# Optimization experiments

Measured on AMD Instinct MI355X. Metric: run time of the kernel, lower is better.

Reference implementation:

```python
import jax, jax.numpy as jnp
import numpy as np

N = 50000   # nodes
E = 800000  # edges (before self-loops)
D = 96      # hidden_dim (= per-head out_channels, concat=False averages heads)
H = 4       # heads
L = 2       # num_layers
NEG_SLOPE = 0.2
EPS_BN = 1e-5


def setup_inputs() -> dict:
    key = jax.random.key(0)
    ks = jax.random.split(key, 8)
    x = jax.random.normal(ks[0], (N, D), dtype=jnp.float32)
    edge_index = jax.random.randint(ks[1], (2, E), 0, N, dtype=jnp.int64)
    # GATConv shared lin: in D -> H*D (per-head dim D), Glorot-ish scale
    W = jax.random.normal(ks[2], (L, D, H * D), dtype=jnp.float32) / np.sqrt(D).astype(np.float32)
    att_src = jax.random.normal(ks[3], (L, H, D), dtype=jnp.float32) * 0.1
    att_dst = jax.random.normal(ks[4], (L, H, D), dtype=jnp.float32) * 0.1
    bias = jnp.zeros((L, D), dtype=jnp.float32)
    gamma = jnp.ones((L, D), dtype=jnp.float32)
    beta = jnp.zeros((L, D), dtype=jnp.float32)
    return dict(x=x, edge_index=edge_index, W=W, att_src=att_src,
                att_dst=att_dst, bias=bias, gamma=gamma, beta=beta)


def _gat_layer(x, src, dst, W, a_src, a_dst, b):
    h = (x @ W).reshape(N, H, D)                      # [N,H,D]
    alpha_src = jnp.einsum('nhd,hd->nh', h, a_src)    # [N,H]
    alpha_dst = jnp.einsum('nhd,hd->nh', h, a_dst)    # [N,H]
    e = jax.nn.leaky_relu(alpha_src[src] + alpha_dst[dst], NEG_SLOPE)  # [Etot,H]
    # edge softmax grouped by destination node (numerically stable)
    m = jax.ops.segment_max(e, dst, num_segments=N)   # [N,H]
    p = jnp.exp(e - m[dst])
    denom = jax.ops.segment_sum(p, dst, num_segments=N)
    alpha = p / (denom[dst] + 1e-16)                  # [Etot,H]
    msg = h[src] * alpha[:, :, None]                  # [Etot,H,D]
    out = jax.ops.segment_sum(msg, dst, num_segments=N)  # [N,H,D]
    return out.mean(axis=1) + b                       # concat=False -> head mean


def reference(x, edge_index, W, att_src, att_dst, bias, gamma, beta):
    # PyG GATConv adds self-loops by default
    loops = jnp.arange(N, dtype=edge_index.dtype)
    ei = jnp.concatenate([edge_index, jnp.stack([loops, loops])], axis=1)
    src, dst = ei[0], ei[1]
    for l in range(L):
        x_res = x
        out = _gat_layer(x, src, dst, W[l], att_src[l], att_dst[l], bias[l])
        # BatchNorm over nodes (training-mode batch statistics, biased var)
        mu = out.mean(axis=0)
        var = out.var(axis=0)
        out = (out - mu) / jnp.sqrt(var + EPS_BN) * gamma[l] + beta[l]
        # dropout is identity at inference
        x = jax.nn.relu(out) + x_res
    return x
```

## Files before the change

kernel.cpp:

```cpp
#include <hip/hip_runtime.h>

#define DD 96
#define HH 4
#define HD 384
#define GN 32
#define NEG_SLOPE 0.2f
#define NB_STATS 128
#define SCAN_BS 1024

typedef unsigned int uint;
typedef unsigned short ushort;

__device__ inline uint pack2bf(float lo, float hi) {
    uint ulo = __float_as_uint(lo); ulo += 0x7fffu + ((ulo >> 16) & 1u);
    uint uhi = __float_as_uint(hi); uhi += 0x7fffu + ((uhi >> 16) & 1u);
    return (ulo >> 16) | (uhi & 0xffff0000u);
}

__global__ void wa_kernel(const float* __restrict__ W, const float* __restrict__ att_src,
                          const float* __restrict__ att_dst, float* __restrict__ wa) {
    const int l = blockIdx.x / DD;
    const int k = blockIdx.x % DD;
    const int t = threadIdx.x;
    const float* Wr = W + ((size_t)l * DD + k) * HD;
    const float* as = att_src + (size_t)l * HD;
    const float* ad = att_dst + (size_t)l * HD;
    const bool hiHalf = t >= 32;
    float s0=0,s1=0,s2=0,s3=0,d0=0,d1=0,d2=0,d3=0;
    int c; float w, ps, pd;
    c = t;       w = Wr[c]; s0 = fmaf(w, as[c], s0); d0 = fmaf(w, ad[c], d0);
    c = t + 64;  w = Wr[c]; ps = w * as[c]; pd = w * ad[c];
    s0 += hiHalf ? 0.f : ps;  s1 += hiHalf ? ps : 0.f;
    d0 += hiHalf ? 0.f : pd;  d1 += hiHalf ? pd : 0.f;
    c = t + 128; w = Wr[c]; s1 = fmaf(w, as[c], s1); d1 = fmaf(w, ad[c], d1);
    c = t + 192; w = Wr[c]; s2 = fmaf(w, as[c], s2); d2 = fmaf(w, ad[c], d2);
    c = t + 256; w = Wr[c]; ps = w * as[c]; pd = w * ad[c];
    s2 += hiHalf ? 0.f : ps;  s3 += hiHalf ? ps : 0.f;
    d2 += hiHalf ? 0.f : pd;  d3 += hiHalf ? pd : 0.f;
    c = t + 320; w = Wr[c]; s3 = fmaf(w, as[c], s3); d3 = fmaf(w, ad[c], d3);
#pragma unroll
    for (int off = 32; off; off >>= 1) {
        s0 += __shfl_xor(s0, off); s1 += __shfl_xor(s1, off);
        s2 += __shfl_xor(s2, off); s3 += __shfl_xor(s3, off);
        d0 += __shfl_xor(d0, off); d1 += __shfl_xor(d1, off);
        d2 += __shfl_xor(d2, off); d3 += __shfl_xor(d3, off);
    }
    if (t == 0) {
        float* o = wa + ((size_t)l * DD + k) * 8;
        o[0]=s0; o[1]=d0; o[2]=s1; o[3]=d1; o[4]=s2; o[5]=d2; o[6]=s3; o[7]=d3;
    }
}

__global__ void __launch_bounds__(256) gemm_kernel(const float* __restrict__ x,
        const float* __restrict__ W, const float* __restrict__ wa,
        uint* __restrict__ hp, float* __restrict__ asrc, float* __restrict__ adst, int N) {
    __shared__ float xs[GN * 100];
    __shared__ float was[DD * 8];
    const int t = threadIdx.x;
    const int n0 = blockIdx.x * GN;
    const int nvalid = min(GN, N - n0);

    for (int i = t; i < DD * 8; i += 256) was[i] = wa[i];
    {
        const float4* xsrc = (const float4*)(x + (size_t)n0 * DD);
        const int lim = (nvalid * DD) / 4;
        for (int i4 = t; i4 < lim; i4 += 256) {
            const float4 v = xsrc[i4];
            const int node = i4 / 24, k = (i4 % 24) * 4;
            float* dp = &xs[node * 100 + k];
            dp[0] = v.x; dp[1] = v.y; dp[2] = v.z; dp[3] = v.w;
        }
    }
    __syncthreads();

    const int lane = t & 63;
    const int nb = (t >> 6) * 8;
    float acc[8][6];
#pragma unroll
    for (int nn = 0; nn < 8; nn++)
#pragma unroll
        for (int j = 0; j < 6; j++) acc[nn][j] = 0.f;

    for (int k = 0; k < DD; k++) {
        float wv[6];
#pragma unroll
        for (int j = 0; j < 6; j++) wv[j] = W[(size_t)k * HD + j * 64 + lane];
#pragma unroll
        for (int nn = 0; nn < 8; nn++) {
            const float xv = xs[(nb + nn) * 100 + k];
#pragma unroll
            for (int j = 0; j < 6; j++) acc[nn][j] = fmaf(xv, wv[j], acc[nn][j]);
        }
    }
#pragma unroll
    for (int nn = 0; nn < 8; nn++) {
        if (nb + nn < nvalid) {
            uint* hr = hp + (size_t)(n0 + nb + nn) * 192;
            hr[lane]       = pack2bf(acc[nn][0], acc[nn][1]);
            hr[64 + lane]  = pack2bf(acc[nn][2], acc[nn][3]);
            hr[128 + lane] = pack2bf(acc[nn][4], acc[nn][5]);
        }
    }
    {
        const int nn = t >> 3, j = t & 7;
        if (nn < nvalid) {
            const float* xr = &xs[nn * 100];
            float s = 0.f;
            for (int k = 0; k < DD; k++) s = fmaf(xr[k], was[k * 8 + j], s);
            const int n = n0 + nn, h = j >> 1;
            if ((j & 1) == 0) asrc[n * 4 + h] = s;
            else              adst[n * 4 + h] = s;
        }
    }
}

__global__ void count_kernel(const int* __restrict__ ei, int* __restrict__ deg, int E) {
    int i = blockIdx.x * blockDim.x + threadIdx.x;
    const int stride = gridDim.x * blockDim.x;
    for (; i < E; i += stride) atomicAdd(&deg[ei[E + i]], 1);
}

__global__ void scan1_kernel(const int* __restrict__ deg, int* __restrict__ locpre,
                             int* __restrict__ bsum, int N) {
    __shared__ int ts[256];
    const int t = threadIdx.x;
    const int base = blockIdx.x * SCAN_BS + t * 4;
    int e0 = 0, e1 = 0, e2 = 0, e3 = 0;
    if (base + 3 < N) {
        const int4 v = *(const int4*)(deg + base);
        e0 = v.x + 1; e1 = v.y + 1; e2 = v.z + 1; e3 = v.w + 1;
    } else {
        if (base     < N) e0 = deg[base]     + 1;
        if (base + 1 < N) e1 = deg[base + 1] + 1;
        if (base + 2 < N) e2 = deg[base + 2] + 1;
        if (base + 3 < N) e3 = deg[base + 3] + 1;
    }
    const int s = e0 + e1 + e2 + e3;
    ts[t] = s;
    __syncthreads();
    for (int off = 1; off < 256; off <<= 1) {
        const int u = (t >= off) ? ts[t - off] : 0;
        __syncthreads();
        ts[t] += u;
        __syncthreads();
    }
    const int ex = ts[t] - s;
    if (base + 3 < N) {
        *(int4*)(locpre + base) = make_int4(ex, ex + e0, ex + e0 + e1, ex + e0 + e1 + e2);
    } else if (base < N) {
        locpre[base] = ex;
        if (base + 1 < N) locpre[base + 1] = ex + e0;
        if (base + 2 < N) locpre[base + 2] = ex + e0 + e1;
    }
    if (t == 255) bsum[blockIdx.x] = ts[255];
}

__global__ void scan2_kernel(int* __restrict__ bsum, int* __restrict__ rowptr,
                             int NBLK, int N) {
    const int t = threadIdx.x;
    const int mine = (t < NBLK) ? bsum[t] : 0;
    int v = mine;
#pragma unroll
    for (int off = 1; off < 64; off <<= 1) {
        const int u = __shfl_up(v, off);
        if (t >= off) v += u;
    }
    if (t < NBLK) bsum[t] = v - mine;
    if (t == 63) rowptr[N] = v;
}

__global__ void scan3_kernel(const int* __restrict__ locpre, const int* __restrict__ bsum,
                             int* __restrict__ rowptr, int* __restrict__ cursor, int N) {
    const int base = blockIdx.x * SCAN_BS + threadIdx.x * 4;
    const int boff = bsum[blockIdx.x];
    if (base + 3 < N) {
        int4 v = *(const int4*)(locpre + base);
        v.x += boff; v.y += boff; v.z += boff; v.w += boff;
        *(int4*)(rowptr + base) = v;
        *(int4*)(cursor + base) = v;
    } else {
        for (int i = base; i < N; i++) {
            const int r = locpre[i] + boff;
            rowptr[i] = r; cursor[i] = r;
        }
    }
}

__global__ void scatter_kernel(const int* __restrict__ ei, int* __restrict__ cursor,
                               const int* __restrict__ rowptr, int* __restrict__ col,
                               int* __restrict__ dstarr, int E, int Etot) {
    int i = blockIdx.x * blockDim.x + threadIdx.x;
    const int stride = gridDim.x * blockDim.x;
    for (; i < Etot; i += stride) {
        if (i < E) {
            const int src = ei[i], dst = ei[E + i];
            const int pos = atomicAdd(&cursor[dst], 1);
            col[pos] = src;
            dstarr[pos] = dst;
        } else {
            const int n = i - E;
            const int pos = rowptr[n + 1] - 1;
            col[pos] = n;
            dstarr[pos] = n;
        }
    }
}

__global__ void ew_kernel(const int* __restrict__ col, const int* __restrict__ dstarr,
                          const float* __restrict__ asrc, const float* __restrict__ adst,
                          float4* __restrict__ ew4, int Etot) {
    int i = blockIdx.x * blockDim.x + threadIdx.x;
    const int stride = gridDim.x * blockDim.x;
    for (; i < Etot; i += stride) {
        const int s = col[i], d = dstarr[i];
        const float4 av = ((const float4*)asrc)[s];
        const float4 dv = ((const float4*)adst)[d];
        float e0 = av.x + dv.x, e1 = av.y + dv.y, e2 = av.z + dv.z, e3 = av.w + dv.w;
        e0 = e0 > 0.f ? e0 : NEG_SLOPE * e0;
        e1 = e1 > 0.f ? e1 : NEG_SLOPE * e1;
        e2 = e2 > 0.f ? e2 : NEG_SLOPE * e2;
        e3 = e3 > 0.f ? e3 : NEG_SLOPE * e3;
        ew4[i] = make_float4(__expf(e0), __expf(e1), __expf(e2), __expf(e3));
    }
}

__global__ void den_kernel(const int* __restrict__ rowptr, const float4* __restrict__ ew4,
                           float4* __restrict__ rden, int N) {
    const int n = blockIdx.x * blockDim.x + threadIdx.x;
    if (n >= N) return;
    const int beg = rowptr[n], endp = rowptr[n + 1];
    float s0 = 0.f, s1 = 0.f, s2 = 0.f, s3 = 0.f;
    for (int i = beg; i < endp; i++) {
        const float4 w = ew4[i];
        s0 += w.x; s1 += w.y; s2 += w.z; s3 += w.w;
    }
    rden[n] = make_float4(0.25f / (s0 + 1e-16f), 0.25f / (s1 + 1e-16f),
                          0.25f / (s2 + 1e-16f), 0.25f / (s3 + 1e-16f));
}

#define EDGE_FMA(u0, u1, u2, w4)                                                      \
    { const float cf1 = hi32 ? w4.y : w4.x;                                           \
      const float cf4 = hi32 ? w4.w : w4.z;                                           \
      acc0 = fmaf(__uint_as_float(u0 << 16), w4.x, acc0);                             \
      acc1 = fmaf(__uint_as_float(u0 & 0xffff0000u), cf1, acc1);                      \
      acc2 = fmaf(__uint_as_float(u1 << 16), w4.y, acc2);                             \
      acc3 = fmaf(__uint_as_float(u1 & 0xffff0000u), w4.z, acc3);                     \
      acc4 = fmaf(__uint_as_float(u2 << 16), cf4, acc4);                              \
      acc5 = fmaf(__uint_as_float(u2 & 0xffff0000u), w4.w, acc5); }

__global__ void agg_csr_kernel(const int* __restrict__ rowptr, const int* __restrict__ col,
                               const uint* __restrict__ hp, const float4* __restrict__ ew4,
                               const float4* __restrict__ rden, const float* __restrict__ bias,
                               float* __restrict__ y, int N) {
    const int lane = threadIdx.x & 63;
    const bool hi32 = lane >= 32;
    const int n = (blockIdx.x * blockDim.x + threadIdx.x) >> 6;
    if (n >= N) return;
    const int beg = rowptr[n], endp = rowptr[n + 1];
    float acc0=0,acc1=0,acc2=0,acc3=0,acc4=0,acc5=0;
    int e = beg;
    for (; e + 4 <= endp; e += 4) {
        const int s0 = col[e], s1 = col[e + 1], s2 = col[e + 2], s3 = col[e + 3];
        const float4 wA = ew4[e],     wB = ew4[e + 1];
        const float4 wC = ew4[e + 2], wD = ew4[e + 3];
        const uint* h0 = hp + (size_t)s0 * 192 + lane;
        const uint* h1 = hp + (size_t)s1 * 192 + lane;
        const uint* h2 = hp + (size_t)s2 * 192 + lane;
        const uint* h3 = hp + (size_t)s3 * 192 + lane;
        const uint u00 = h0[0], u01 = h0[64], u02 = h0[128];
        const uint u10 = h1[0], u11 = h1[64], u12 = h1[128];
        const uint u20 = h2[0], u21 = h2[64], u22 = h2[128];
        const uint u30 = h3[0], u31 = h3[64], u32 = h3[128];
        EDGE_FMA(u00, u01, u02, wA);
        EDGE_FMA(u10, u11, u12, wB);
        EDGE_FMA(u20, u21, u22, wC);
        EDGE_FMA(u30, u31, u32, wD);
    }
    for (; e < endp; e++) {
        const int s0 = col[e];
        const float4 wA = ew4[e];
        const uint* h0 = hp + (size_t)s0 * 192 + lane;
        const uint u00 = h0[0], u01 = h0[64], u02 = h0[128];
        EDGE_FMA(u00, u01, u02, wA);
    }
    const float4 rd = rden[n];
    const float rc1 = hi32 ? rd.y : rd.x;
    const float rc4 = hi32 ? rd.w : rd.z;
    const float A = acc0 * rd.x + acc3 * rd.z;
    const float B = acc1 * rc1  + acc4 * rc4;
    const float C = acc2 * rd.y + acc5 * rd.w;
    const float shB = __shfl_xor(B, 32);
    const float shC = __shfl_xor(C, 32);
    float* yr = y + (size_t)n * DD;
    yr[lane] = A + (hi32 ? shC : shB) + bias[lane];
    if (!hi32) yr[64 + lane] = B + shC + bias[64 + lane];
}

__global__ void bnstats_kernel(const float* __restrict__ y, float* __restrict__ pbuf,
                               int total4) {
    __shared__ float ps[384 * 4];
    __shared__ float qs[384 * 4];
    const int t = threadIdx.x;
    const int stride = gridDim.x * 384;
    float s0=0,s1=0,s2=0,s3=0,q0=0,q1=0,q2=0,q3=0;
    for (int i = blockIdx.x * 384 + t; i < total4; i += stride) {
        const float4 v = ((const float4*)y)[i];
        s0 += v.x; q0 = fmaf(v.x, v.x, q0);
        s1 += v.y; q1 = fmaf(v.y, v.y, q1);
        s2 += v.z; q2 = fmaf(v.z, v.z, q2);
        s3 += v.w; q3 = fmaf(v.w, v.w, q3);
    }
    ps[t*4+0]=s0; ps[t*4+1]=s1; ps[t*4+2]=s2; ps[t*4+3]=s3;
    qs[t*4+0]=q0; qs[t*4+1]=q1; qs[t*4+2]=q2; qs[t*4+3]=q3;
    __syncthreads();
    if (t < 192) {
        const int d = t % 96;
        const float* src = (t < 96) ? ps : qs;
        float r = 0.f;
#pragma unroll
        for (int m = 0; m < 16; m++) r += src[d + 96 * m];
        pbuf[blockIdx.x * 192 + t] = r;
    }
}

__global__ void bnfin_kernel(const float* __restrict__ pbuf, const float* __restrict__ gamma,
                             const float* __restrict__ beta, float* __restrict__ scsh, int N) {
    const int d = threadIdx.x;
    float s = 0.f, q = 0.f;
    for (int b = 0; b < NB_STATS; b++) {
        s += pbuf[b * 192 + d];
        q += pbuf[b * 192 + 96 + d];
    }
    const float invN = 1.f / (float)N;
    const float mu = s * invN;
    const float var = q * invN - mu * mu;
    const float sc = gamma[d] * rsqrtf(var + 1e-5f);
    scsh[d] = sc;
    scsh[d + DD] = beta[d] - mu * sc;
}

__global__ void bn_apply_kernel(const float* __restrict__ y, const float* __restrict__ scsh,
                                const float* __restrict__ xin, float* __restrict__ xout,
                                int total4) {
    int i = blockIdx.x * blockDim.x + threadIdx.x;
    const int stride = gridDim.x * blockDim.x;
    for (; i < total4; i += stride) {
        const int d4 = (i % 24) * 4;
        const float4 v = ((const float4*)y)[i];
        const float4 xi = ((const float4*)xin)[i];
        float4 o; float a;
        a = fmaf(v.x, scsh[d4],     scsh[d4 + DD]);     o.x = (a > 0.f ? a : 0.f) + xi.x;
        a = fmaf(v.y, scsh[d4 + 1], scsh[d4 + 1 + DD]); o.y = (a > 0.f ? a : 0.f) + xi.y;
        a = fmaf(v.z, scsh[d4 + 2], scsh[d4 + 2 + DD]); o.z = (a > 0.f ? a : 0.f) + xi.z;
        a = fmaf(v.w, scsh[d4 + 3], scsh[d4 + 3 + DD]); o.w = (a > 0.f ? a : 0.f) + xi.w;
        ((float4*)xout)[i] = o;
    }
}

extern "C" void kernel_launch(void* const* d_in, const int* in_sizes, int n_in,
                              void* d_out, int out_size, void* d_ws, size_t ws_size,
                              hipStream_t stream) {
    const float* x        = (const float*)d_in[0];
    const int*   ei       = (const int*)d_in[1];
    const float* W        = (const float*)d_in[2];
    const float* att_src  = (const float*)d_in[3];
    const float* att_dst  = (const float*)d_in[4];
    const float* bias     = (const float*)d_in[5];
    const float* gamma    = (const float*)d_in[6];
    const float* beta     = (const float*)d_in[7];
    float* out_final = (float*)d_out;

    const int N = in_sizes[0] / DD;
    const int E = in_sizes[1] / 2;
    const int Etot = E + N;
    const int NBLK = (N + SCAN_BS - 1) / SCAN_BS;

    char* ws = (char*)d_ws;
    size_t off = 0;
    auto alloc = [&](size_t bytes) -> void* {
        void* p = ws + off;
        off += (bytes + 255) & ~(size_t)255;
        return p;
    };
    uint*   hp     = (uint*)alloc((size_t)N * 192 * 4);
    float*  asrc   = (float*)alloc((size_t)N * HH * 4);
    float*  adst   = (float*)alloc((size_t)N * HH * 4);
    float*  y      = (float*)alloc((size_t)N * DD * 4);
    float*  xbuf   = (float*)alloc((size_t)N * DD * 4);
    float*  pbuf   = (float*)alloc((size_t)NB_STATS * 192 * 4);
    float*  scsh   = (float*)alloc(2 * DD * 4);
    float*  wa     = (float*)alloc(2 * DD * 8 * 4);
    int*    deg    = (int*)alloc((size_t)N * 4);
    int*    locpre = (int*)alloc((size_t)N * 4);
    int*    bsum   = (int*)alloc(64 * 4);
    int*    rowptr = (int*)alloc((size_t)(N + 1) * 4);
    int*    cursor = (int*)alloc((size_t)N * 4);
    int*    colidx = (int*)alloc((size_t)Etot * 4);
    int*    dstarr = (int*)alloc((size_t)Etot * 4);
    float4* ew4    = (float4*)alloc((size_t)Etot * 16);
    float4* rden   = (float4*)alloc((size_t)N * 16);

    hipMemsetAsync(deg, 0, (size_t)N * 4, stream);
    count_kernel<<<1024, 256, 0, stream>>>(ei, deg, E);
    scan1_kernel<<<NBLK, 256, 0, stream>>>(deg, locpre, bsum, N);
    scan2_kernel<<<1, 64, 0, stream>>>(bsum, rowptr, NBLK, N);
    scan3_kernel<<<NBLK, 256, 0, stream>>>(locpre, bsum, rowptr, cursor, N);
    scatter_kernel<<<1024, 256, 0, stream>>>(ei, cursor, rowptr, colidx, dstarr, E, Etot);
    wa_kernel<<<2 * DD, 64, 0, stream>>>(W, att_src, att_dst, wa);

    for (int l = 0; l < 2; l++) {
        const float* xin = (l == 0) ? x : xbuf;
        float* xout = (l == 1) ? out_final : xbuf;

        gemm_kernel<<<(N + GN - 1) / GN, 256, 0, stream>>>(
            xin, W + (size_t)l * DD * HD, wa + (size_t)l * DD * 8, hp, asrc, adst, N);
        ew_kernel<<<2048, 256, 0, stream>>>(colidx, dstarr, asrc, adst, ew4, Etot);
        den_kernel<<<(N + 255) / 256, 256, 0, stream>>>(rowptr, ew4, rden, N);
        agg_csr_kernel<<<(N * 64 + 255) / 256, 256, 0, stream>>>(
            rowptr, colidx, hp, ew4, rden, bias + (size_t)l * DD, y, N);
        bnstats_kernel<<<NB_STATS, 384, 0, stream>>>(y, pbuf, N * DD / 4);
        bnfin_kernel<<<1, DD, 0, stream>>>(pbuf, gamma + (size_t)l * DD,
                                           beta + (size_t)l * DD, scsh, N);
        bn_apply_kernel<<<2048, 256, 0, stream>>>(y, scsh, xin, xout, N * DD / 4);
    }
}
```

Baseline: 485.6 us.

## Fuse softmax denominator into aggregation and store bf16 features as contiguous triples

Removes the separate den_kernel: each aggregation wavefront now sums the edge weights itself while it gathers, so the per-node normalizer is computed in registers and the rden buffer and one launch per layer go away. The packed bf16 feature layout changes from three strided words per lane to three contiguous words per lane, written and read as a single 12-byte vector access. The gather loop unroll grows from 4 to 8 edges so more loads are in flight. The costs are redundant denominator adds across all 64 lanes, higher register pressure, and possibly less efficient unaligned 12-byte vector loads.

```diff
diff --git a/kernel.cpp b/kernel.cpp
--- a/kernel.cpp
+++ b/kernel.cpp
@@ -10,6 +10,9 @@
 
 typedef unsigned int uint;
 typedef unsigned short ushort;
+
+typedef uint uint3v __attribute__((ext_vector_type(3)));
+typedef uint3v __attribute__((aligned(4))) uint3a;
 
 __device__ inline uint pack2bf(float lo, float hi) {
     uint ulo = __float_as_uint(lo); ulo += 0x7fffu + ((ulo >> 16) & 1u);
@@ -95,10 +98,12 @@
 #pragma unroll
     for (int nn = 0; nn < 8; nn++) {
         if (nb + nn < nvalid) {
-            uint* hr = hp + (size_t)(n0 + nb + nn) * 192;
-            hr[lane]       = pack2bf(acc[nn][0], acc[nn][1]);
-            hr[64 + lane]  = pack2bf(acc[nn][2], acc[nn][3]);
-            hr[128 + lane] = pack2bf(acc[nn][4], acc[nn][5]);
+            uint* hr = hp + (size_t)(n0 + nb + nn) * 192 + lane * 3;
+            uint3v v;
+            v.x = pack2bf(acc[nn][0], acc[nn][1]);
+            v.y = pack2bf(acc[nn][2], acc[nn][3]);
+            v.z = pack2bf(acc[nn][4], acc[nn][5]);
+            *(uint3a*)hr = v;
         }
     }
     {
@@ -224,33 +229,20 @@
     }
 }
 
-__global__ void den_kernel(const int* __restrict__ rowptr, const float4* __restrict__ ew4,
-                           float4* __restrict__ rden, int N) {
-    const int n = blockIdx.x * blockDim.x + threadIdx.x;
-    if (n >= N) return;
-    const int beg = rowptr[n], endp = rowptr[n + 1];
-    float s0 = 0.f, s1 = 0.f, s2 = 0.f, s3 = 0.f;
-    for (int i = beg; i < endp; i++) {
-        const float4 w = ew4[i];
-        s0 += w.x; s1 += w.y; s2 += w.z; s3 += w.w;
-    }
-    rden[n] = make_float4(0.25f / (s0 + 1e-16f), 0.25f / (s1 + 1e-16f),
-                          0.25f / (s2 + 1e-16f), 0.25f / (s3 + 1e-16f));
-}
-
-#define EDGE_FMA(u0, u1, u2, w4)                                                      \
-    { const float cf1 = hi32 ? w4.y : w4.x;                                           \
+#define EDGE_FMA(u, w4)                                                               \
+    { den0 += w4.x; den1 += w4.y; den2 += w4.z; den3 += w4.w;                         \
+      const float cf1 = hi32 ? w4.y : w4.x;                                           \
       const float cf4 = hi32 ? w4.w : w4.z;                                           \
-      acc0 = fmaf(__uint_as_float(u0 << 16), w4.x, acc0);                             \
-      acc1 = fmaf(__uint_as_float(u0 & 0xffff0000u), cf1, acc1);                      \
-      acc2 = fmaf(__uint_as_float(u1 << 16), w4.y, acc2);                             \
-      acc3 = fmaf(__uint_as_float(u1 & 0xffff0000u), w4.z, acc3);                     \
-      acc4 = fmaf(__uint_as_float(u2 << 16), cf4, acc4);                              \
-      acc5 = fmaf(__uint_as_float(u2 & 0xffff0000u), w4.w, acc5); }
+      acc0 = fmaf(__uint_as_float(u.x << 16), w4.x, acc0);                            \
+      acc1 = fmaf(__uint_as_float(u.x & 0xffff0000u), cf1, acc1);                     \
+      acc2 = fmaf(__uint_as_float(u.y << 16), w4.y, acc2);                            \
+      acc3 = fmaf(__uint_as_float(u.y & 0xffff0000u), w4.z, acc3);                    \
+      acc4 = fmaf(__uint_as_float(u.z << 16), cf4, acc4);                             \
+      acc5 = fmaf(__uint_as_float(u.z & 0xffff0000u), w4.w, acc5); }
 
 __global__ void agg_csr_kernel(const int* __restrict__ rowptr, const int* __restrict__ col,
                                const uint* __restrict__ hp, const float4* __restrict__ ew4,
-                               const float4* __restrict__ rden, const float* __restrict__ bias,
+                               const float* __restrict__ bias,
                                float* __restrict__ y, int N) {
     const int lane = threadIdx.x & 63;
     const bool hi32 = lane >= 32;
@@ -258,37 +250,37 @@
     if (n >= N) return;
     const int beg = rowptr[n], endp = rowptr[n + 1];
     float acc0=0,acc1=0,acc2=0,acc3=0,acc4=0,acc5=0;
+    float den0=0,den1=0,den2=0,den3=0;
     int e = beg;
-    for (; e + 4 <= endp; e += 4) {
-        const int s0 = col[e], s1 = col[e + 1], s2 = col[e + 2], s3 = col[e + 3];
-        const float4 wA = ew4[e],     wB = ew4[e + 1];
-        const float4 wC = ew4[e + 2], wD = ew4[e + 3];
-        const uint* h0 = hp + (size_t)s0 * 192 + lane;
-        const uint* h1 = hp + (size_t)s1 * 192 + lane;
-        const uint* h2 = hp + (size_t)s2 * 192 + lane;
-        const uint* h3 = hp + (size_t)s3 * 192 + lane;
-        const uint u00 = h0[0], u01 = h0[64], u02 = h0[128];
-        const uint u10 = h1[0], u11 = h1[64], u12 = h1[128];
-        const uint u20 = h2[0], u21 = h2[64], u22 = h2[128];
-        const uint u30 = h3[0], u31 = h3[64], u32 = h3[128];
-        EDGE_FMA(u00, u01, u02, wA);
-        EDGE_FMA(u10, u11, u12, wB);
-        EDGE_FMA(u20, u21, u22, wC);
-        EDGE_FMA(u30, u31, u32, wD);
+    for (; e + 8 <= endp; e += 8) {
+        int s[8];
+#pragma unroll
+        for (int k = 0; k < 8; k++) s[k] = col[e + k];
+        uint3v u[8];
+#pragma unroll
+        for (int k = 0; k < 8; k++)
+            u[k] = *(const uint3a*)(hp + (size_t)s[k] * 192 + lane * 3);
+        float4 w[8];
+#pragma unroll
+        for (int k = 0; k < 8; k++) w[k] = ew4[e + k];
+#pragma unroll
+        for (int k = 0; k < 8; k++) EDGE_FMA(u[k], w[k]);
     }
     for (; e < endp; e++) {
         const int s0 = col[e];
         const float4 wA = ew4[e];
-        const uint* h0 = hp + (size_t)s0 * 192 + lane;
-        const uint u00 = h0[0], u01 = h0[64], u02 = h0[128];
-        EDGE_FMA(u00, u01, u02, wA);
-    }
-    const float4 rd = rden[n];
-    const float rc1 = hi32 ? rd.y : rd.x;
-    const float rc4 = hi32 ? rd.w : rd.z;
-    const float A = acc0 * rd.x + acc3 * rd.z;
-    const float B = acc1 * rc1  + acc4 * rc4;
-    const float C = acc2 * rd.y + acc5 * rd.w;
+        const uint3v u0 = *(const uint3a*)(hp + (size_t)s0 * 192 + lane * 3);
+        EDGE_FMA(u0, wA);
+    }
+    const float r0 = 0.25f / (den0 + 1e-16f);
+    const float r1 = 0.25f / (den1 + 1e-16f);
+    const float r2 = 0.25f / (den2 + 1e-16f);
+    const float r3 = 0.25f / (den3 + 1e-16f);
+    const float rc1 = hi32 ? r1 : r0;
+    const float rc4 = hi32 ? r3 : r2;
+    const float A = acc0 * r0 + acc3 * r2;
+    const float B = acc1 * rc1 + acc4 * rc4;
+    const float C = acc2 * r1 + acc5 * r3;
     const float shB = __shfl_xor(B, 32);
     const float shC = __shfl_xor(C, 32);
     float* yr = y + (size_t)n * DD;
@@ -398,7 +390,6 @@
     int*    colidx = (int*)alloc((size_t)Etot * 4);
     int*    dstarr = (int*)alloc((size_t)Etot * 4);
     float4* ew4    = (float4*)alloc((size_t)Etot * 16);
-    float4* rden   = (float4*)alloc((size_t)N * 16);
 
     hipMemsetAsync(deg, 0, (size_t)N * 4, stream);
     count_kernel<<<1024, 256, 0, stream>>>(ei, deg, E);
@@ -415,9 +406,8 @@
         gemm_kernel<<<(N + GN - 1) / GN, 256, 0, stream>>>(
             xin, W + (size_t)l * DD * HD, wa + (size_t)l * DD * 8, hp, asrc, adst, N);
         ew_kernel<<<2048, 256, 0, stream>>>(colidx, dstarr, asrc, adst, ew4, Etot);
-        den_kernel<<<(N + 255) / 256, 256, 0, stream>>>(rowptr, ew4, rden, N);
         agg_csr_kernel<<<(N * 64 + 255) / 256, 256, 0, stream>>>(
-            rowptr, colidx, hp, ew4, rden, bias + (size_t)l * DD, y, N);
+            rowptr, colidx, hp, ew4, bias + (size_t)l * DD, y, N);
         bnstats_kernel<<<NB_STATS, 384, 0, stream>>>(y, pbuf, N * DD / 4);
         bnfin_kernel<<<1, DD, 0, stream>>>(pbuf, gamma + (size_t)l * DD,
                                            beta + (size_t)l * DD, scsh, N);
```

Result: no change. 491.3 us (+1.2%).

## Use bf16 MFMA for node projection GEMM and fuse softmax denominator into aggregation

Applied to the files above, without the earlier changes.

Replaces the scalar FP32 shared-memory GEMM with a bf16 MFMA 16x16x32 kernel. A new kernel pre-transposes W and appends the attention-projected vectors as extra columns, so the attention logits come out of the same matrix multiply. It also removes the separate denominator kernel by accumulating the per-head softmax sums inside the CSR aggregation loop. The cost is lower precision: x and W are rounded to bf16 before the multiply, which also affects the attention logits. The MFMA kernel keeps 25 accumulator tiles per wave, which puts register pressure on occupancy.

```diff
diff --git a/kernel.cpp b/kernel.cpp
--- a/kernel.cpp
+++ b/kernel.cpp
@@ -3,18 +3,25 @@
 #define DD 96
 #define HH 4
 #define HD 384
-#define GN 32
 #define NEG_SLOPE 0.2f
 #define NB_STATS 128
 #define SCAN_BS 1024
+#define WTC 400
 
 typedef unsigned int uint;
 typedef unsigned short ushort;
+typedef __attribute__((ext_vector_type(8))) short bf16x8;
+typedef __attribute__((ext_vector_type(4))) float f32x4;
 
 __device__ inline uint pack2bf(float lo, float hi) {
     uint ulo = __float_as_uint(lo); ulo += 0x7fffu + ((ulo >> 16) & 1u);
     uint uhi = __float_as_uint(hi); uhi += 0x7fffu + ((uhi >> 16) & 1u);
     return (ulo >> 16) | (uhi & 0xffff0000u);
+}
+__device__ inline ushort f2bf(float f) {
+    uint u = __float_as_uint(f);
+    u += 0x7fffu + ((u >> 16) & 1u);
+    return (ushort)(u >> 16);
 }
 
 __global__ void wa_kernel(const float* __restrict__ W, const float* __restrict__ att_src,
@@ -51,65 +58,64 @@
     }
 }
 
-__global__ void __launch_bounds__(256) gemm_kernel(const float* __restrict__ x,
-        const float* __restrict__ W, const float* __restrict__ wa,
-        uint* __restrict__ hp, float* __restrict__ asrc, float* __restrict__ adst, int N) {
-    __shared__ float xs[GN * 100];
-    __shared__ float was[DD * 8];
+__global__ void wt_kernel(const float* __restrict__ W, const float* __restrict__ wa,
+                          ushort* __restrict__ wt) {
+    const int l = blockIdx.x / WTC;
+    const int c = blockIdx.x % WTC;
+    const int k = threadIdx.x;
+    float v = 0.f;
+    if (c < HD)        v = W[((size_t)l * DD + k) * HD + c];
+    else if (c < HD+8) v = wa[((size_t)l * DD + k) * 8 + (c - HD)];
+    wt[((size_t)l * WTC + c) * DD + k] = f2bf(v);
+}
+
+__global__ void __launch_bounds__(256) gemm_mfma_kernel(const float* __restrict__ x,
+        const ushort* __restrict__ wt, uint* __restrict__ hp,
+        float* __restrict__ asrc, float* __restrict__ adst, int N) {
     const int t = threadIdx.x;
-    const int n0 = blockIdx.x * GN;
-    const int nvalid = min(GN, N - n0);
-
-    for (int i = t; i < DD * 8; i += 256) was[i] = wa[i];
-    {
-        const float4* xsrc = (const float4*)(x + (size_t)n0 * DD);
-        const int lim = (nvalid * DD) / 4;
-        for (int i4 = t; i4 < lim; i4 += 256) {
-            const float4 v = xsrc[i4];
-            const int node = i4 / 24, k = (i4 % 24) * 4;
-            float* dp = &xs[node * 100 + k];
-            dp[0] = v.x; dp[1] = v.y; dp[2] = v.z; dp[3] = v.w;
+    const int w = t >> 6;
+    const int lane = t & 63;
+    const int q = lane & 15, g = lane >> 4;
+    const int base = blockIdx.x * 64 + w * 16;
+    const int nA = min(base + q, N - 1);
+
+    f32x4 acc[25];
+#pragma unroll
+    for (int i = 0; i < 25; i++) acc[i] = (f32x4){0.f, 0.f, 0.f, 0.f};
+
+#pragma unroll
+    for (int s = 0; s < 3; s++) {
+        const float* xp = x + (size_t)nA * DD + s * 32 + g * 8;
+        const float4 xa = *(const float4*)xp;
+        const float4 xb = *(const float4*)(xp + 4);
+        union { uint u[4]; bf16x8 v; } A;
+        A.u[0] = pack2bf(xa.x, xa.y);
+        A.u[1] = pack2bf(xa.z, xa.w);
+        A.u[2] = pack2bf(xb.x, xb.y);
+        A.u[3] = pack2bf(xb.z, xb.w);
+#pragma unroll
+        for (int tt = 0; tt < 25; tt++) {
+            const ushort* wp = wt + (size_t)(tt * 16 + q) * DD + s * 32 + g * 8;
+            union { uint4 u4; bf16x8 v; } B;
+            B.u4 = *(const uint4*)wp;
+            acc[tt] = __builtin_amdgcn_mfma_f32_16x16x32_bf16(A.v, B.v, acc[tt], 0, 0, 0);
         }
     }
-    __syncthreads();
-
-    const int lane = t & 63;
-    const int nb = (t >> 6) * 8;
-    float acc[8][6];
-#pragma unroll
-    for (int nn = 0; nn < 8; nn++)
-#pragma unroll
-        for (int j = 0; j < 6; j++) acc[nn][j] = 0.f;
-
-    for (int k = 0; k < DD; k++) {
-        float wv[6];
-#pragma unroll
-        for (int j = 0; j < 6; j++) wv[j] = W[(size_t)k * HD + j * 64 + lane];
-#pragma unroll
-        for (int nn = 0; nn < 8; nn++) {
-            const float xv = xs[(nb + nn) * 100 + k];
-#pragma unroll
-            for (int j = 0; j < 6; j++) acc[nn][j] = fmaf(xv, wv[j], acc[nn][j]);
-        }
-    }
-#pragma unroll
-    for (int nn = 0; nn < 8; nn++) {
-        if (nb + nn < nvalid) {
-            uint* hr = hp + (size_t)(n0 + nb + nn) * 192;
-            hr[lane]       = pack2bf(acc[nn][0], acc[nn][1]);
-            hr[64 + lane]  = pack2bf(acc[nn][2], acc[nn][3]);
-            hr[128 + lane] = pack2bf(acc[nn][4], acc[nn][5]);
-        }
-    }
-    {
-        const int nn = t >> 3, j = t & 7;
-        if (nn < nvalid) {
-            const float* xr = &xs[nn * 100];
-            float s = 0.f;
-            for (int k = 0; k < DD; k++) s = fmaf(xr[k], was[k * 8 + j], s);
-            const int n = n0 + nn, h = j >> 1;
-            if ((j & 1) == 0) asrc[n * 4 + h] = s;
-            else              adst[n * 4 + h] = s;
+#pragma unroll
+    for (int r = 0; r < 4; r++) {
+        const int node = base + g * 4 + r;
+        if (node < N) {
+            uint* hr = hp + (size_t)node * 192;
+#pragma unroll
+            for (int p = 0; p < 3; p++)
+#pragma unroll
+                for (int tt = 0; tt < 4; tt++)
+                    hr[p * 64 + tt * 16 + q] = pack2bf(acc[p * 8 + tt][r], acc[p * 8 + tt + 4][r]);
+            if (q < 8) {
+                const float v = acc[24][r];
+                if ((q & 1) == 0) asrc[node * 4 + (q >> 1)] = v;
+                else              adst[node * 4 + (q >> 1)] = v;
+            }
         }
     }
 }
@@ -224,22 +230,9 @@
     }
 }
 
-__global__ void den_kernel(const int* __restrict__ rowptr, const float4* __restrict__ ew4,
-                           float4* __restrict__ rden, int N) {
-    const int n = blockIdx.x * blockDim.x + threadIdx.x;
-    if (n >= N) return;
-    const int beg = rowptr[n], endp = rowptr[n + 1];
-    float s0 = 0.f, s1 = 0.f, s2 = 0.f, s3 = 0.f;
-    for (int i = beg; i < endp; i++) {
-        const float4 w = ew4[i];
-        s0 += w.x; s1 += w.y; s2 += w.z; s3 += w.w;
-    }
-    rden[n] = make_float4(0.25f / (s0 + 1e-16f), 0.25f / (s1 + 1e-16f),
-                          0.25f / (s2 + 1e-16f), 0.25f / (s3 + 1e-16f));
-}
-
 #define EDGE_FMA(u0, u1, u2, w4)                                                      \
-    { const float cf1 = hi32 ? w4.y : w4.x;                                           \
+    { den0 += w4.x; den1 += w4.y; den2 += w4.z; den3 += w4.w;                         \
+      const float cf1 = hi32 ? w4.y : w4.x;                                           \
       const float cf4 = hi32 ? w4.w : w4.z;                                           \
       acc0 = fmaf(__uint_as_float(u0 << 16), w4.x, acc0);                             \
       acc1 = fmaf(__uint_as_float(u0 & 0xffff0000u), cf1, acc1);                      \
@@ -250,7 +243,7 @@
 
 __global__ void agg_csr_kernel(const int* __restrict__ rowptr, const int* __restrict__ col,
                                const uint* __restrict__ hp, const float4* __restrict__ ew4,
-                               const float4* __restrict__ rden, const float* __restrict__ bias,
+                               const float* __restrict__ bias,
                                float* __restrict__ y, int N) {
     const int lane = threadIdx.x & 63;
     const bool hi32 = lane >= 32;
@@ -258,6 +251,7 @@
     if (n >= N) return;
     const int beg = rowptr[n], endp = rowptr[n + 1];
     float acc0=0,acc1=0,acc2=0,acc3=0,acc4=0,acc5=0;
+    float den0=0,den1=0,den2=0,den3=0;
     int e = beg;
     for (; e + 4 <= endp; e += 4) {
         const int s0 = col[e], s1 = col[e + 1], s2 = col[e + 2], s3 = col[e + 3];
@@ -283,12 +277,15 @@
         const uint u00 = h0[0], u01 = h0[64], u02 = h0[128];
         EDGE_FMA(u00, u01, u02, wA);
     }
-    const float4 rd = rden[n];
-    const float rc1 = hi32 ? rd.y : rd.x;
-    const float rc4 = hi32 ? rd.w : rd.z;
-    const float A = acc0 * rd.x + acc3 * rd.z;
-    const float B = acc1 * rc1  + acc4 * rc4;
-    const float C = acc2 * rd.y + acc5 * rd.w;
+    const float r0 = 0.25f / (den0 + 1e-16f);
+    const float r1 = 0.25f / (den1 + 1e-16f);
+    const float r2 = 0.25f / (den2 + 1e-16f);
+    const float r3 = 0.25f / (den3 + 1e-16f);
+    const float rc1 = hi32 ? r1 : r0;
+    const float rc4 = hi32 ? r3 : r2;
+    const float A = acc0 * r0 + acc3 * r2;
+    const float B = acc1 * rc1 + acc4 * rc4;
+    const float C = acc2 * r1 + acc5 * r3;
     const float shB = __shfl_xor(B, 32);
     const float shC = __shfl_xor(C, 32);
     float* yr = y + (size_t)n * DD;
@@ -390,6 +387,7 @@
     float*  pbuf   = (float*)alloc((size_t)NB_STATS * 192 * 4);
     float*  scsh   = (float*)alloc(2 * DD * 4);
     float*  wa     = (float*)alloc(2 * DD * 8 * 4);
+    ushort* wt     = (ushort*)alloc((size_t)2 * WTC * DD * 2);
     int*    deg    = (int*)alloc((size_t)N * 4);
     int*    locpre = (int*)alloc((size_t)N * 4);
     int*    bsum   = (int*)alloc(64 * 4);
@@ -398,7 +396,6 @@
     int*    colidx = (int*)alloc((size_t)Etot * 4);
     int*    dstarr = (int*)alloc((size_t)Etot * 4);
     float4* ew4    = (float4*)alloc((size_t)Etot * 16);
-    float4* rden   = (float4*)alloc((size_t)N * 16);
 
     hipMemsetAsync(deg, 0, (size_t)N * 4, stream);
     count_kernel<<<1024, 256, 0, stream>>>(ei, deg, E);
@@ -407,17 +404,17 @@
     scan3_kernel<<<NBLK, 256, 0, stream>>>(locpre, bsum, rowptr, cursor, N);
     scatter_kernel<<<1024, 256, 0, stream>>>(ei, cursor, rowptr, colidx, dstarr, E, Etot);
     wa_kernel<<<2 * DD, 64, 0, stream>>>(W, att_src, att_dst, wa);
+    wt_kernel<<<2 * WTC, DD, 0, stream>>>(W, wa, wt);
 
     for (int l = 0; l < 2; l++) {
         const float* xin = (l == 0) ? x : xbuf;
         float* xout = (l == 1) ? out_final : xbuf;
 
-        gemm_kernel<<<(N + GN - 1) / GN, 256, 0, stream>>>(
-            xin, W + (size_t)l * DD * HD, wa + (size_t)l * DD * 8, hp, asrc, adst, N);
+        gemm_mfma_kernel<<<(N + 63) / 64, 256, 0, stream>>>(
+            xin, wt + (size_t)l * WTC * DD, hp, asrc, adst, N);
         ew_kernel<<<2048, 256, 0, stream>>>(colidx, dstarr, asrc, adst, ew4, Etot);
-        den_kernel<<<(N + 255) / 256, 256, 0, stream>>>(rowptr, ew4, rden, N);
         agg_csr_kernel<<<(N * 64 + 255) / 256, 256, 0, stream>>>(
-            rowptr, colidx, hp, ew4, rden, bias + (size_t)l * DD, y, N);
+            rowptr, colidx, hp, ew4, bias + (size_t)l * DD, y, N);
         bnstats_kernel<<<NB_STATS, 384, 0, stream>>>(y, pbuf, N * DD / 4);
         bnfin_kernel<<<1, DD, 0, stream>>>(pbuf, gamma + (size_t)l * DD,
                                            beta + (size_t)l * DD, scsh, N);
```

Result: faster. 396.4 us (-18.4%).
